# Optimization experiments

Hardware: AMD Instinct MI355X
Metric: run time of the kernel (lower is better)

Reference implementation:

```python
import jax, jax.numpy as jnp
import numpy as np

DIM = 768
HEADS = 12
HEAD_DIM = DIM // HEADS  # 64
SCALE = HEAD_DIM ** -0.5
B, H, W = 16, 64, 64
EPS_BN = 1e-5
EPS_SQRT = 1e-5


def setup_inputs() -> dict:
    key = jax.random.key(0)
    k0, k1, k2, k3, k4 = jax.random.split(key, 5)
    x = jax.random.normal(k0, (B, DIM, H, W), dtype=jnp.float32)
    # 1x1 conv == pointwise matmul over channels
    qkv_w = jax.random.normal(k1, (3 * DIM, DIM), dtype=jnp.float32) * (DIM ** -0.5)
    qkv_b = jax.random.normal(k2, (3 * DIM,), dtype=jnp.float32) * 0.01
    gamma = 1.0 + 0.1 * jax.random.normal(k3, (DIM,), dtype=jnp.float32)
    beta = 0.1 * jax.random.normal(k4, (DIM,), dtype=jnp.float32)
    return {"x": x, "qkv_w": qkv_w, "qkv_b": qkv_b, "gamma": gamma, "beta": beta}


def reference(x, qkv_w, qkv_b, gamma, beta):
    b, c, h, w = x.shape
    n = h * w
    xf = x.reshape(b, c, n)  # [B, C, N]
    # qkv 1x1 conv
    qkv = jnp.einsum('oc,bcn->bon', qkv_w, xf) + qkv_b[None, :, None]  # [B, 3C, N]
    qkv = qkv.reshape(b, 3, HEADS, HEAD_DIM, n)
    q, k, v = qkv[:, 0], qkv[:, 1], qkv[:, 2]  # each [B, h, d, N]
    # channel attention: contract over N -> [B, h, d, d]
    attn = jnp.einsum('bhdn,bhen->bhde', q, k) * SCALE
    attn = jnp.sign(attn) * jnp.sqrt(jnp.abs(attn) + EPS_SQRT)
    attn = jax.nn.softmax(attn, axis=-1)
    # BatchNorm2d (training-mode batch statistics, biased variance) + ReLU
    mean = jnp.mean(x, axis=(0, 2, 3))
    var = jnp.var(x, axis=(0, 2, 3))
    y = (x - mean[None, :, None, None]) * jax.lax.rsqrt(var + EPS_BN)[None, :, None, None]
    y = y * gamma[None, :, None, None] + beta[None, :, None, None]
    out = jnp.maximum(y, 0.0)
    # original module discards attn; returned here so the attention math is
    return out, attn
```

## Files before the change

kernel.cpp:

```cpp
#include <hip/hip_runtime.h>
#include <hip/hip_bf16.h>

#define DIM 768
#define NB 16
#define NPOS 4096
#define HEADS 12

typedef unsigned short u16;
typedef __attribute__((ext_vector_type(4))) float f32x4;
typedef __attribute__((ext_vector_type(8))) short s16x8;
typedef __attribute__((ext_vector_type(4))) u16 u16x4;

static __device__ __forceinline__ u16 f2bf(float f) {
  __hip_bfloat16 h = __float2bfloat16(f);
  u16 u; __builtin_memcpy(&u, &h, 2); return u;
}
static __device__ __forceinline__ float bf2f(u16 u) {
  unsigned int x = ((unsigned int)u) << 16;
  float f; __builtin_memcpy(&f, &x, 4); return f;
}

static __device__ __forceinline__ void load_lds16(const void* g, void* l) {
  __builtin_amdgcn_global_load_lds(
      (const __attribute__((address_space(1))) unsigned int*)g,
      (__attribute__((address_space(3))) unsigned int*)l, 16, 0, 0);
}

static __device__ __forceinline__ int lds_idx(int row, int slotf) {
  return row * 64 + (((slotf) ^ (row & 7)) << 3);
}


__global__ __launch_bounds__(128) void sums_cast_kernel(const float* __restrict__ x,
                                                        float* __restrict__ sum_bc,
                                                        float* __restrict__ sumsq_bc,
                                                        u16* __restrict__ Xb) {
  int bc = blockIdx.x;
  const float4* p = (const float4*)(x + (size_t)bc * NPOS);
  u16x4* ob = (u16x4*)(Xb + (size_t)bc * NPOS);
  int t = threadIdx.x;
  float s = 0.f, ss = 0.f;
  for (int i = t; i < NPOS / 4; i += 128) {
    float4 v = p[i];
    s  += v.x + v.y + v.z + v.w;
    ss += v.x * v.x + v.y * v.y + v.z * v.z + v.w * v.w;
    u16x4 hv = {f2bf(v.x), f2bf(v.y), f2bf(v.z), f2bf(v.w)};
    ob[i] = hv;
  }
  for (int off = 32; off; off >>= 1) { s += __shfl_down(s, off); ss += __shfl_down(ss, off); }
  __shared__ float red[4];
  int lane = t & 63, w = t >> 6;
  if (lane == 0) { red[w] = s; red[2 + w] = ss; }
  __syncthreads();
  if (t == 0) { sum_bc[bc] = red[0] + red[1]; sumsq_bc[bc] = red[2] + red[3]; }
}

__global__ void finalize_kernel(const float* __restrict__ sum_bc, const float* __restrict__ sumsq_bc,
                                const float* __restrict__ gamma, const float* __restrict__ beta,
                                float* __restrict__ chanScale, float* __restrict__ chanShift) {
  int c = blockIdx.x * blockDim.x + threadIdx.x;
  if (c >= DIM) return;
  float s = 0.f, ss = 0.f;
  for (int b = 0; b < NB; b++) { s += sum_bc[b * DIM + c]; ss += sumsq_bc[b * DIM + c]; }
  const float invn = 1.f / ((float)NB * (float)NPOS);
  float mean = s * invn;
  float var  = ss * invn - mean * mean;
  float rstd = rsqrtf(var + 1e-5f);
  float a = rstd * gamma[c];
  chanScale[c] = a;
  chanShift[c] = beta[c] - mean * a;
}

__global__ __launch_bounds__(256) void bn_kernel(const float* __restrict__ x,
                                                 const float* __restrict__ chanScale,
                                                 const float* __restrict__ chanShift,
                                                 float* __restrict__ out) {
  const size_t n4 = (size_t)NB * DIM * NPOS / 4;
  const float4* x4 = (const float4*)x;
  float4* o4 = (float4*)out;
  for (size_t i = (size_t)blockIdx.x * blockDim.x + threadIdx.x; i < n4;
       i += (size_t)gridDim.x * blockDim.x) {
    float4 v = x4[i];
    int c = (int)((i >> 10) % DIM);
    float a = chanScale[c], sh = chanShift[c];
    v.x = fmaxf(fmaf(v.x, a, sh), 0.f);
    v.y = fmaxf(fmaf(v.y, a, sh), 0.f);
    v.z = fmaxf(fmaf(v.z, a, sh), 0.f);
    v.w = fmaxf(fmaf(v.w, a, sh), 0.f);
    o4[i] = v;
  }
}


__global__ __launch_bounds__(64) void tvecw_kernel(const float* __restrict__ W,
                                                   const float* __restrict__ sum_bc,
                                                   float* __restrict__ tvec,
                                                   u16* __restrict__ Wb) {
  int r = blockIdx.x;
  int lane = threadIdx.x;
  const float* wr = W + (size_t)r * DIM;
  float acc[NB];
#pragma unroll
  for (int b = 0; b < NB; b++) acc[b] = 0.f;
#pragma unroll
  for (int j = 0; j < DIM / 64; j++) {
    int c = lane + j * 64;
    float wv = wr[c];
    Wb[(size_t)r * DIM + c] = f2bf(wv);
#pragma unroll
    for (int b = 0; b < NB; b++) acc[b] += wv * sum_bc[b * DIM + c];
  }
#pragma unroll
  for (int b = 0; b < NB; b++) {
    float v = acc[b];
    for (int off = 32; off; off >>= 1) v += __shfl_down(v, off);
    if (lane == 0) tvec[(size_t)b * 1536 + r] = v;
  }
}


template <bool SYMM>
__global__ __launch_bounds__(256) void gemm_kernel(
    const u16* __restrict__ A, long long strideA,
    const u16* __restrict__ B, long long strideB,
    u16* __restrict__ C, long long strideC,
    int lda, int ldb, int ldc, int K, int nGram,
    const u16* __restrict__ XbBn, const float* __restrict__ chanScale,
    const float* __restrict__ chanShift, float* __restrict__ outY) {
  __shared__ __align__(16) u16 As[2][128 * 64];
  __shared__ __align__(16) u16 Bs[2][128 * 64];

  int ti, tj, bz;
  if (SYMM) {
    if ((int)blockIdx.x >= nGram) {
      int t = threadIdx.x;
      const size_t total8 = (size_t)NB * DIM * NPOS / 8;
      size_t stride = (size_t)(gridDim.x - nGram) * 256;
      const s16x8* xs = (const s16x8*)XbBn;
      float4* o4 = (float4*)outY;
      for (size_t i = (size_t)(blockIdx.x - nGram) * 256 + t; i < total8; i += stride) {
        s16x8 v = xs[i];
        int c = (int)((i >> 9) % DIM);
        float a = chanScale[c], sh = chanShift[c];
        float4 o0, o1;
        o0.x = fmaxf(fmaf(bf2f((u16)v[0]), a, sh), 0.f);
        o0.y = fmaxf(fmaf(bf2f((u16)v[1]), a, sh), 0.f);
        o0.z = fmaxf(fmaf(bf2f((u16)v[2]), a, sh), 0.f);
        o0.w = fmaxf(fmaf(bf2f((u16)v[3]), a, sh), 0.f);
        o1.x = fmaxf(fmaf(bf2f((u16)v[4]), a, sh), 0.f);
        o1.y = fmaxf(fmaf(bf2f((u16)v[5]), a, sh), 0.f);
        o1.z = fmaxf(fmaf(bf2f((u16)v[6]), a, sh), 0.f);
        o1.w = fmaxf(fmaf(bf2f((u16)v[7]), a, sh), 0.f);
        o4[2 * i] = o0;
        o4[2 * i + 1] = o1;
      }
      return;
    }
    int bid = blockIdx.x;
    int swz = (bid & 7) * 42 + (bid >> 3);
    bz = swz / 21;
    int idx = swz % 21, rem = 6;
    ti = 0;
    while (idx >= rem) { idx -= rem; ti++; rem--; }
    tj = ti + idx;
  } else {
    ti = blockIdx.x; tj = blockIdx.y; bz = blockIdx.z;
  }
  const u16* Ab = A + (size_t)bz * strideA;
  const u16* Bb = B + (size_t)bz * strideB;
  u16* Cb = C + (size_t)bz * strideC;
  int ib = ti * 128, jb = tj * 128;

  int t = threadIdx.x, lane = t & 63, w = t >> 6;
  int wr = (w >> 1) * 64, wc = (w & 1) * 64;
  int fr = lane & 15, q4 = lane >> 4;
  int srow = lane >> 3;
  int sslot = (lane & 7) ^ srow;

  const u16* Asrc = Ab + (size_t)(ib + srow) * lda + sslot * 8;
  const u16* Bsrc = Bb + (size_t)(jb + srow) * ldb + sslot * 8;

  f32x4 acc[4][4];
#pragma unroll
  for (int m = 0; m < 4; m++)
#pragma unroll
    for (int n = 0; n < 4; n++) acc[m][n] = (f32x4){0.f, 0.f, 0.f, 0.f};

#define STAGE(buf, k0)                                                          \
  {                                                                             \
    _Pragma("unroll")                                                           \
    for (int i = 0; i < 4; i++) {                                               \
      int q = w * 4 + i;                                                        \
      load_lds16(Asrc + (size_t)(q * 8) * lda + (k0), (char*)As[buf] + q * 1024);\
      load_lds16(Bsrc + (size_t)(q * 8) * ldb + (k0), (char*)Bs[buf] + q * 1024);\
    }                                                                           \
  }

#define COMPUTE(buf)                                                            \
  {                                                                             \
    _Pragma("unroll")                                                           \
    for (int kk = 0; kk < 2; kk++) {                                            \
      int sbase = kk * 4 + q4;                                                  \
      s16x8 af[4], bfv[4];                                                      \
      _Pragma("unroll")                                                         \
      for (int m = 0; m < 4; m++) af[m] = *(const s16x8*)&As[buf][lds_idx(wr + m * 16 + fr, sbase)]; \
      _Pragma("unroll")                                                         \
      for (int n = 0; n < 4; n++) bfv[n] = *(const s16x8*)&Bs[buf][lds_idx(wc + n * 16 + fr, sbase)]; \
      _Pragma("unroll")                                                         \
      for (int m = 0; m < 4; m++)                                               \
        _Pragma("unroll")                                                       \
        for (int n = 0; n < 4; n++)                                             \
          acc[m][n] = __builtin_amdgcn_mfma_f32_16x16x32_bf16(af[m], bfv[n], acc[m][n], 0, 0, 0); \
    }                                                                           \
  }

  STAGE(0, 0);
  __syncthreads();
  for (int k0 = 0; k0 < K; k0 += 128) {
    STAGE(1, k0 + 64);
    COMPUTE(0);
    __syncthreads();
    if (k0 + 128 < K) STAGE(0, k0 + 128);
    COMPUTE(1);
    __syncthreads();
  }
#undef STAGE
#undef COMPUTE

  int rbase = q4 * 4;
#pragma unroll
  for (int m = 0; m < 4; m++)
#pragma unroll
    for (int n = 0; n < 4; n++)
#pragma unroll
      for (int r = 0; r < 4; r++) {
        int row = ib + wr + m * 16 + rbase + r;
        int col = jb + wc + n * 16 + fr;
        u16 v = f2bf(acc[m][n][r]);
        Cb[(size_t)row * ldc + col] = v;
        if (SYMM && ti != tj) Cb[(size_t)col * ldc + row] = v;
      }
}


__global__ __launch_bounds__(256) void attn_kernel(const u16* __restrict__ Pb,
                                                   const u16* __restrict__ Wb,
                                                   const float* __restrict__ bias,
                                                   const float* __restrict__ tvec,
                                                   float* __restrict__ outAttn) {
  int h = blockIdx.x, b = blockIdx.y;
  __shared__ __align__(16) u16 As[2][64 * 64];
  __shared__ __align__(16) u16 Bs[2][64 * 64];
  __shared__ float sm[64 * 65];
  const u16* Pa = Pb + ((size_t)b * DIM + h * 64) * DIM;
  const u16* Wk = Wb + (size_t)(DIM + h * 64) * DIM;

  int t = threadIdx.x, lane = t & 63, w = t >> 6;
  int fr = lane & 15, q4 = lane >> 4;
  int srow = lane >> 3;
  int sslot = (lane & 7) ^ srow;

  const u16* Asrc = Pa + (size_t)srow * DIM + sslot * 8;
  const u16* Bsrc = Wk + (size_t)srow * DIM + sslot * 8;

  f32x4 acc[4];
#pragma unroll
  for (int n = 0; n < 4; n++) acc[n] = (f32x4){0.f, 0.f, 0.f, 0.f};

#define ASTAGE(buf, k0)                                                          \
  {                                                                              \
    _Pragma("unroll")                                                            \
    for (int i = 0; i < 2; i++) {                                                \
      int q = w * 2 + i;                                                         \
      load_lds16(Asrc + (size_t)(q * 8) * DIM + (k0), (char*)As[buf] + q * 1024);\
      load_lds16(Bsrc + (size_t)(q * 8) * DIM + (k0), (char*)Bs[buf] + q * 1024);\
    }                                                                            \
  }

#define ACOMPUTE(buf)                                                            \
  {                                                                              \
    _Pragma("unroll")                                                            \
    for (int kk = 0; kk < 2; kk++) {                                             \
      int sbase = kk * 4 + q4;                                                   \
      s16x8 af = *(const s16x8*)&As[buf][lds_idx(w * 16 + fr, sbase)];           \
      _Pragma("unroll")                                                          \
      for (int n = 0; n < 4; n++) {                                              \
        s16x8 bfv = *(const s16x8*)&Bs[buf][lds_idx(n * 16 + fr, sbase)];        \
        acc[n] = __builtin_amdgcn_mfma_f32_16x16x32_bf16(af, bfv, acc[n], 0, 0, 0); \
      }                                                                          \
    }                                                                            \
  }

  ASTAGE(0, 0);
  __syncthreads();
  for (int k0 = 0; k0 < DIM; k0 += 128) {
    ASTAGE(1, k0 + 64);
    ACOMPUTE(0);
    __syncthreads();
    if (k0 + 128 < DIM) ASTAGE(0, k0 + 128);
    ACOMPUTE(1);
    __syncthreads();
  }
#undef ASTAGE
#undef ACOMPUTE

  const float* tq = tvec + (size_t)b * 1536 + h * 64;
  const float* tk = tq + DIM;
  const float* bq = bias + h * 64;
  const float* bk = bias + DIM + h * 64;
  int rbase = q4 * 4;
#pragma unroll
  for (int n = 0; n < 4; n++) {
    int e = n * 16 + fr;
    float bke = bk[e], tke = tk[e];
#pragma unroll
    for (int r = 0; r < 4; r++) {
      int d = w * 16 + rbase + r;
      float bqd = bq[d];
      float raw = acc[n][r] + bqd * tke + bke * tq[d] + 4096.f * bqd * bke;
      float val = 0.125f * raw;
      float sq = sqrtf(fabsf(val) + 1e-5f);
      sm[d * 65 + e] = val > 0.f ? sq : (val < 0.f ? -sq : 0.f);
    }
  }
  __syncthreads();
  {
    int d = t >> 2, qd = (t & 3) * 16;
    const float* row = &sm[d * 65];
    float mx = -1e30f;
#pragma unroll
    for (int e2 = 0; e2 < 16; e2++) mx = fmaxf(mx, row[qd + e2]);
    mx = fmaxf(mx, __shfl_xor(mx, 1));
    mx = fmaxf(mx, __shfl_xor(mx, 2));
    float sum = 0.f;
#pragma unroll
    for (int e2 = 0; e2 < 16; e2++) sum += __expf(row[qd + e2] - mx);
    sum += __shfl_xor(sum, 1);
    sum += __shfl_xor(sum, 2);
    float inv = 1.f / sum;
    float* o = outAttn + (((size_t)b * HEADS + h) * 64 + d) * 64;
#pragma unroll
    for (int e2 = 0; e2 < 16; e2++) o[qd + e2] = __expf(row[qd + e2] - mx) * inv;
  }
}


extern "C" void kernel_launch(void* const* d_in, const int* in_sizes, int n_in,
                              void* d_out, int out_size, void* d_ws, size_t ws_size,
                              hipStream_t stream) {
  const float* x     = (const float*)d_in[0];
  const float* qkv_w = (const float*)d_in[1];
  const float* qkv_b = (const float*)d_in[2];
  const float* gamma = (const float*)d_in[3];
  const float* beta  = (const float*)d_in[4];
  float* out = (float*)d_out;
  float* ws  = (float*)d_ws;

  float* sum_bc    = ws;
  float* sumsq_bc  = ws + 12288;
  float* chanScale = ws + 24576;
  float* chanShift = ws + 25344;
  float* tvec      = ws + 26112;
  u16* Wb = (u16*)(ws + 50688);
  u16* Gb = (u16*)((char*)d_ws + 2562048);
  u16* Pb = (u16*)((char*)d_ws + 2562048 + 18874368);

  const bool wsRoom = ws_size >= (41943040ull + 100663296ull + 1024ull);
  u16* Xb = wsRoom ? (u16*)((char*)d_ws + 41943040) : (u16*)d_out;

  sums_cast_kernel<<<NB * DIM, 128, 0, stream>>>(x, sum_bc, sumsq_bc, Xb);
  finalize_kernel<<<3, 256, 0, stream>>>(sum_bc, sumsq_bc, gamma, beta, chanScale, chanShift);
  tvecw_kernel<<<2 * DIM, 64, 0, stream>>>(qkv_w, sum_bc, tvec, Wb);

  if (wsRoom) {
    gemm_kernel<true><<<336 + 256, 256, 0, stream>>>(
        Xb, (long long)DIM * NPOS, Xb, (long long)DIM * NPOS, Gb, (long long)DIM * DIM,
        NPOS, NPOS, DIM, NPOS, 336, Xb, chanScale, chanShift, out);
  } else {
    gemm_kernel<true><<<336, 256, 0, stream>>>(
        Xb, (long long)DIM * NPOS, Xb, (long long)DIM * NPOS, Gb, (long long)DIM * DIM,
        NPOS, NPOS, DIM, NPOS, 336, nullptr, chanScale, chanShift, nullptr);
    bn_kernel<<<2048, 256, 0, stream>>>(x, chanScale, chanShift, out);
  }

  gemm_kernel<false><<<dim3(6, 6, NB), 256, 0, stream>>>(
      Wb, 0LL, Gb, (long long)DIM * DIM, Pb, (long long)DIM * DIM,
      DIM, DIM, DIM, DIM, 1 << 30, nullptr, nullptr, nullptr, nullptr);

  attn_kernel<<<dim3(HEADS, NB), 256, 0, stream>>>(Pb, Wb, qkv_b, tvec,
                                                   out + (size_t)NB * DIM * NPOS);
}
```

Measured before the change: 276.0 us.

## Replace full syncthreads with partial vmcnt waits in GEMM double-buffer loops

Both MFMA GEMM kernels replace __syncthreads, which drains all outstanding global-to-LDS loads, with explicit s_waitcnt vmcnt(N) that waits only for the older stage's loads, followed by raw s_barrier and sched_barrier. The next stage's prefetch can then stay in flight while the current buffer is computed. The cost is correctness that depends on the exact count of outstanding vector memory ops per stage, so a compiler-inserted load or a changed stage size could break synchronisation.

```diff
diff --git a/kernel.cpp b/kernel.cpp
--- a/kernel.cpp
+++ b/kernel.cpp
@@ -190,7 +190,7 @@
   {                                                                             \
     _Pragma("unroll")                                                           \
     for (int i = 0; i < 4; i++) {                                               \
-      int q = w * 4 + i;                                                        \
+      int q = w * 4 + i;             \
       load_lds16(Asrc + (size_t)(q * 8) * lda + (k0), (char*)As[buf] + q * 1024);\
       load_lds16(Bsrc + (size_t)(q * 8) * ldb + (k0), (char*)Bs[buf] + q * 1024);\
     }                                                                           \
@@ -214,15 +214,25 @@
     }                                                                           \
   }
 
+  const int nt = K >> 6;
   STAGE(0, 0);
-  __syncthreads();
-  for (int k0 = 0; k0 < K; k0 += 128) {
-    STAGE(1, k0 + 64);
+  for (int t2 = 0; t2 < nt; t2 += 2) {
+    STAGE(1, (t2 + 1) << 6);
+    asm volatile("s_waitcnt vmcnt(8)" ::: "memory");
+    __builtin_amdgcn_s_barrier();
+    __builtin_amdgcn_sched_barrier(0);
     COMPUTE(0);
-    __syncthreads();
-    if (k0 + 128 < K) STAGE(0, k0 + 128);
+    __builtin_amdgcn_s_barrier();
+    if (t2 + 2 < nt) {
+      STAGE(0, (t2 + 2) << 6);
+      asm volatile("s_waitcnt vmcnt(8)" ::: "memory");
+    } else {
+      asm volatile("s_waitcnt vmcnt(0)" ::: "memory");
+    }
+    __builtin_amdgcn_s_barrier();
+    __builtin_amdgcn_sched_barrier(0);
     COMPUTE(1);
-    __syncthreads();
+    __builtin_amdgcn_s_barrier();
   }
 #undef STAGE
 #undef COMPUTE
@@ -271,7 +281,7 @@
   {                                                                              \
     _Pragma("unroll")                                                            \
     for (int i = 0; i < 2; i++) {                                                \
-      int q = w * 2 + i;                                                         \
+      int q = w * 2 + i;              \
       load_lds16(Asrc + (size_t)(q * 8) * DIM + (k0), (char*)As[buf] + q * 1024);\
       load_lds16(Bsrc + (size_t)(q * 8) * DIM + (k0), (char*)Bs[buf] + q * 1024);\
     }                                                                            \
@@ -292,14 +302,23 @@
   }
 
   ASTAGE(0, 0);
-  __syncthreads();
-  for (int k0 = 0; k0 < DIM; k0 += 128) {
-    ASTAGE(1, k0 + 64);
+  for (int t2 = 0; t2 < 12; t2 += 2) {
+    ASTAGE(1, (t2 + 1) << 6);
+    asm volatile("s_waitcnt vmcnt(4)" ::: "memory");
+    __builtin_amdgcn_s_barrier();
+    __builtin_amdgcn_sched_barrier(0);
     ACOMPUTE(0);
-    __syncthreads();
-    if (k0 + 128 < DIM) ASTAGE(0, k0 + 128);
+    __builtin_amdgcn_s_barrier();
+    if (t2 + 2 < 12) {
+      ASTAGE(0, (t2 + 2) << 6);
+      asm volatile("s_waitcnt vmcnt(4)" ::: "memory");
+    } else {
+      asm volatile("s_waitcnt vmcnt(0)" ::: "memory");
+    }
+    __builtin_amdgcn_s_barrier();
+    __builtin_amdgcn_sched_barrier(0);
     ACOMPUTE(1);
-    __syncthreads();
+    __builtin_amdgcn_s_barrier();
   }
 #undef ASTAGE
 #undef ACOMPUTE
```

Result: faster. 270.6 us (-2.0%).
